# Performance work log

Measured on AMD Instinct MI355X. Metric: run time of the kernel, lower is better.

Reference implementation:

```python
import jax, jax.numpy as jnp
import numpy as np

W = 801  # wavelength grid points
B = 16384  # batch of thickness stacks


def setup_inputs() -> dict:
    key = jax.random.key(0)
    k1, = jax.random.split(key, 1)
    # 7 physical film thicknesses in nm, uniform in [0, 200)
    d_phys = jax.random.uniform(k1, (B, 7), dtype=jnp.float32) * 200.0
    # wavelength grid in nm (docstring: spectrum length 801)
    lam = jnp.linspace(400.0, 800.0, W, dtype=jnp.float32)
    # material refractive indices (module default fallbacks, complex n + ik)
    n_Si = jnp.full((W,), 4.0 + 0.0j, dtype=jnp.complex64)
    n_SiO2 = jnp.full((W,), 1.46 + 0.0j, dtype=jnp.complex64)
    n_Si3N4 = jnp.full((W,), 2.0 + 0.0j, dtype=jnp.complex64)
    return {"d_phys": d_phys, "n_Si": n_Si, "n_SiO2": n_SiO2,
            "n_Si3N4": n_Si3N4, "lam": lam}


def reference(d_phys, n_Si, n_SiO2, n_Si3N4, lam):
    # Transfer-matrix reflectometry for stack:
    # Air | SiO2 | Si3N4 | SiO2 | Si3N4 | SiO2 | Si3N4 | SiO2 | Si
    k0 = (2.0 * jnp.pi) / lam  # [W]
    b = d_phys.shape[0]
    n_Air = jnp.ones_like(n_Si)
    layers_n = [n_Air, n_SiO2, n_Si3N4, n_SiO2, n_Si3N4,
                n_SiO2, n_Si3N4, n_SiO2, n_Si]
    zeros = jnp.zeros((b, 1), dtype=d_phys.dtype)
    d_list = [zeros] + [d_phys[:, i:i + 1] for i in range(7)] + [zeros]

    M00 = jnp.ones((b, lam.shape[0]), dtype=jnp.complex64)
    M11 = jnp.ones_like(M00)
    M01 = jnp.zeros_like(M00)
    M10 = jnp.zeros_like(M00)

    N_curr = layers_n[0]
    n_layers = len(layers_n)
    for i in range(1, n_layers):  # fixed 8-step recurrence over interfaces
        N_next = layers_n[i]
        d_next = d_list[i]  # [b, 1] real
        sum_n = N_curr + N_next  # [W]
        sub_n = N_curr - N_next
        r = sub_n / sum_n            # Fresnel reflection coeff [W]
        inv_t = sum_n / (2.0 * N_curr)  # 1/transmission [W]
        m00 = (M00 + M01 * r) * inv_t
        m01 = (M00 * r + M01) * inv_t
        m10 = (M10 + M11 * r) * inv_t
        m11 = (M10 * r + M11) * inv_t
        M00, M01, M10, M11 = m00, m01, m10, m11
        if i < n_layers - 1:
            phi = k0[None, :] * N_next[None, :] * d_next.astype(jnp.complex64)  # [b, W]
            P = jnp.exp(-1j * phi)
            Pi = jnp.exp(1j * phi)
            M00 = M00 * P
            M01 = M01 * Pi
            M10 = M10 * P
            M11 = M11 * Pi
        N_curr = N_next

    r_final = M10 / M00
    R = jnp.abs(r_final) ** 2  # real reflectance spectrum [b, W]
    return R
```

## Files before the change

### kernel.cpp

```cpp
#include <hip/hip_runtime.h>

#define WPTS 801
#define ROWS 4
#define NT 256

struct c2 { float x, y; };

__device__ __forceinline__ c2 c_addc(c2 a, c2 b) { return {a.x + b.x, a.y + b.y}; }
__device__ __forceinline__ c2 c_subc(c2 a, c2 b) { return {a.x - b.x, a.y - b.y}; }
__device__ __forceinline__ c2 c_divc(c2 a, c2 b) {
    float inv = 1.0f / (b.x * b.x + b.y * b.y);
    return {(a.x * b.x + a.y * b.y) * inv, (a.y * b.x - a.x * b.y) * inv};
}

__global__ __launch_bounds__(NT)
void kla_tmm_kernel(const float* __restrict__ d_phys,
                    const float* __restrict__ nSi_f,
                    const float* __restrict__ nSiO2_f,
                    const float* __restrict__ nSi3N4_f,
                    const float* __restrict__ lam,
                    float* __restrict__ out,
                    int B)
{
    const int nRowBlks = (B + ROWS - 1) / ROWS;
    const int t = blockIdx.x * NT + threadIdx.x;
    if (t >= nRowBlks * WPTS) return;

    const int w = t % WPTS;
    const int row0 = (t / WPTS) * ROWS;
    const int nrows = min(ROWS, B - row0);

    const bool ilv = (nSiO2_f[1] == 0.0f);
    float nSx, nSy, nOx, nOy, nNx, nNy;
    if (ilv) {
        nSx = nSi_f[2 * w];    nSy = nSi_f[2 * w + 1];
        nOx = nSiO2_f[2 * w];  nOy = nSiO2_f[2 * w + 1];
        nNx = nSi3N4_f[2 * w]; nNy = nSi3N4_f[2 * w + 1];
    } else {
        nSx = nSi_f[w];    nSy = 0.0f;
        nOx = nSiO2_f[w];  nOy = 0.0f;
        nNx = nSi3N4_f[w]; nNy = 0.0f;
    }

    const bool realn = (nOy == 0.0f) && (nNy == 0.0f) && (nSy == 0.0f);

    if (realn && nrows == ROWS) {
        const float rlam = __builtin_amdgcn_rcpf(lam[w]);
        const float kOr = nOx * rlam;
        const float kNr = nNx * rlam;
        const float gAO = __builtin_amdgcn_rcpf(nOx);
        const float gON = nOx * __builtin_amdgcn_rcpf(nNx);
        const float gNO = nNx * gAO;

        const float* base = d_phys + (size_t)row0 * 7;
        float* orow = out + (size_t)row0 * WPTS + w;

        #pragma unroll
        for (int rr = 0; rr < ROWS; ++rr) {
            const float* dd = base + (size_t)rr * 7;
            float v0x = nOx, v0y = 0.0f;
            float v1x = nSx, v1y = 0.0f;

            #pragma unroll
            for (int i = 7; i >= 1; --i) {
                const float nu = dd[i - 1] * ((i & 1) ? kOr : kNr);
                const float s = __builtin_amdgcn_sinf(nu);
                const float c = __builtin_amdgcn_cosf(nu);
                const float w0x = v0x * c + v1y * s;
                const float w0y = v0y * c - v1x * s;
                const float w1x = v1x * c + v0y * s;
                const float w1y = v1y * c - v0x * s;
                const float g = (i == 1) ? gAO : ((i & 1) ? gNO : gON);
                v0x = w0x * g;
                v0y = w0y * g;
                v1x = w1x;
                v1y = w1y;
            }

            const float ax = v0x - v1x, ay = v0y - v1y;
            const float bx = v0x + v1x, by = v0y + v1y;
            const float num = ax * ax + ay * ay;
            const float den = bx * bx + by * by;
            orow[(size_t)rr * WPTS] = num * __builtin_amdgcn_rcpf(den);
        }
    } else {
        const float k0 = 6.28318530717958647692f / lam[w];
        const c2 nA = {1.0f, 0.0f};
        const c2 nO = {nOx, nOy}, nN = {nNx, nNy}, nS = {nSx, nSy};
        const c2 rAO  = c_divc(c_subc(nA, nO), c_addc(nA, nO));
        const c2 rON  = c_divc(c_subc(nO, nN), c_addc(nO, nN));
        const c2 rNO  = {-rON.x, -rON.y};
        const c2 rOSi = c_divc(c_subc(nO, nS), c_addc(nO, nS));
        const c2 kO = {k0 * nO.x, k0 * nO.y};
        const c2 kN = {k0 * nN.x, k0 * nN.y};

        for (int rr = 0; rr < nrows; ++rr) {
            const int row = row0 + rr;
            const float* dd = d_phys + (size_t)row * 7;

            c2 u0 = {1.0f, 0.0f};
            c2 u1 = rOSi;

            #pragma unroll
            for (int i = 7; i >= 1; --i) {
                const float d = dd[i - 1];
                const c2 kk = (i & 1) ? kO : kN;
                const float alpha = kk.x * d;
                const float beta  = kk.y * d;
                float s, c;
                __sincosf(alpha, &s, &c);
                const float ep = __expf(beta);
                const float em = __expf(-beta);

                c2 v;
                v.x = ep * (u0.x * c + u0.y * s);
                v.y = ep * (u0.y * c - u0.x * s);
                u0 = v;
                v.x = em * (u1.x * c - u1.y * s);
                v.y = em * (u1.y * c + u1.x * s);
                u1 = v;

                const c2 ri = (i == 1) ? rAO : ((i & 1) ? rNO : rON);
                c2 w0, w1;
                w0.x = u0.x + ri.x * u1.x - ri.y * u1.y;
                w0.y = u0.y + ri.x * u1.y + ri.y * u1.x;
                w1.x = u1.x + ri.x * u0.x - ri.y * u0.y;
                w1.y = u1.y + ri.x * u0.y + ri.y * u0.x;
                u0 = w0; u1 = w1;
            }

            out[(size_t)row * WPTS + w] =
                (u1.x * u1.x + u1.y * u1.y) / (u0.x * u0.x + u0.y * u0.y);
        }
    }
}

extern "C" void kernel_launch(void* const* d_in, const int* in_sizes, int n_in,
                              void* d_out, int out_size, void* d_ws, size_t ws_size,
                              hipStream_t stream) {
    const float* d_phys  = (const float*)d_in[0];
    const float* nSi     = (const float*)d_in[1];
    const float* nSiO2   = (const float*)d_in[2];
    const float* nSi3N4  = (const float*)d_in[3];
    const float* lam     = (const float*)d_in[4];
    float* out = (float*)d_out;

    const int B = in_sizes[0] / 7;
    const int nRowBlks = (B + ROWS - 1) / ROWS;
    const int nTasks = nRowBlks * WPTS;
    const int grid = (nTasks + NT - 1) / NT;

    kla_tmm_kernel<<<grid, NT, 0, stream>>>(
        d_phys, nSi, nSiO2, nSi3N4, lam, out, B);
}
```

Measured before the change: 47.40 us.

## Compute transfer-matrix recurrence in packed fp16 with polynomial sin/cos

```diff
diff --git a/kernel.cpp b/kernel.cpp
--- a/kernel.cpp
+++ b/kernel.cpp
@@ -3,6 +3,8 @@
 #define WPTS 801
 #define ROWS 4
 #define NT 256
+
+typedef _Float16 h2 __attribute__((ext_vector_type(2)));
 
 struct c2 { float x, y; };
 
@@ -11,6 +13,10 @@
 __device__ __forceinline__ c2 c_divc(c2 a, c2 b) {
     float inv = 1.0f / (b.x * b.x + b.y * b.y);
     return {(a.x * b.x + a.y * b.y) * inv, (a.y * b.x - a.x * b.y) * inv};
+}
+
+__device__ __forceinline__ h2 h2bcast(float v) {
+    h2 r; r.x = (_Float16)v; r.y = (_Float16)v; return r;
 }
 
 __global__ __launch_bounds__(NT)
@@ -46,42 +52,86 @@
 
     if (realn && nrows == ROWS) {
         const float rlam = __builtin_amdgcn_rcpf(lam[w]);
-        const float kOr = nOx * rlam;
-        const float kNr = nNx * rlam;
+        const float kO2 = 2.0f * nOx * rlam;
+        const float kN2 = 2.0f * nNx * rlam;
         const float gAO = __builtin_amdgcn_rcpf(nOx);
         const float gON = nOx * __builtin_amdgcn_rcpf(nNx);
         const float gNO = nNx * gAO;
 
+        const h2 hgAO = h2bcast(gAO);
+        const h2 hgON = h2bcast(gON);
+        const h2 hgNO = h2bcast(gNO);
+
+        const h2 hA1 = h2bcast( 3.14159265f);
+        const h2 hA3 = h2bcast(-5.16771278f);
+        const h2 hA5 = h2bcast( 2.55016404f);
+        const h2 hA7 = h2bcast(-0.59926453f);
+        const h2 hC2 = h2bcast(-4.93480220f);
+        const h2 hC4 = h2bcast( 4.05871213f);
+        const h2 hC6 = h2bcast(-1.33526277f);
+        const h2 hOne = h2bcast(1.0f);
+
+        const h2 v0init = h2bcast(nOx);
+        const h2 v1init = h2bcast(nSx);
+
         const float* base = d_phys + (size_t)row0 * 7;
         float* orow = out + (size_t)row0 * WPTS + w;
 
         #pragma unroll
-        for (int rr = 0; rr < ROWS; ++rr) {
-            const float* dd = base + (size_t)rr * 7;
-            float v0x = nOx, v0y = 0.0f;
-            float v1x = nSx, v1y = 0.0f;
+        for (int pr = 0; pr < ROWS; pr += 2) {
+            const float* dA = base + (size_t)pr * 7;
+            const float* dB = dA + 7;
+
+            h2 v0x = v0init, v0y = h2bcast(0.0f);
+            h2 v1x = v1init, v1y = h2bcast(0.0f);
 
             #pragma unroll
             for (int i = 7; i >= 1; --i) {
-                const float nu = dd[i - 1] * ((i & 1) ? kOr : kNr);
-                const float s = __builtin_amdgcn_sinf(nu);
-                const float c = __builtin_amdgcn_cosf(nu);
-                const float w0x = v0x * c + v1y * s;
-                const float w0y = v0y * c - v1x * s;
-                const float w1x = v1x * c + v0y * s;
-                const float w1y = v1y * c - v0x * s;
-                const float g = (i == 1) ? gAO : ((i & 1) ? gNO : gON);
-                v0x = w0x * g;
-                v0y = w0y * g;
-                v1x = w1x;
-                v1y = w1y;
-            }
-
-            const float ax = v0x - v1x, ay = v0y - v1y;
-            const float bx = v0x + v1x, by = v0y + v1y;
-            const float num = ax * ax + ay * ay;
-            const float den = bx * bx + by * by;
-            orow[(size_t)rr * WPTS] = num * __builtin_amdgcn_rcpf(den);
+                const float kk = (i & 1) ? kO2 : kN2;
+                const h2 hg = (i == 1) ? hgAO : ((i & 1) ? hgNO : hgON);
+
+                const float nuA = dA[i - 1] * kk;
+                const float nuB = dB[i - 1] * kk;
+                const float tA = nuA - __builtin_rintf(nuA);
+                const float tB = nuB - __builtin_rintf(nuB);
+                h2 tt; tt.x = (_Float16)tA; tt.y = (_Float16)tB;
+
+                h2 q = tt * tt;
+                h2 ps = hA5 + q * hA7;
+                ps = hA3 + q * ps;
+                ps = hA1 + q * ps;
+                h2 s = tt * ps;
+                h2 pc = hC4 + q * hC6;
+                pc = hC2 + q * pc;
+                h2 c = hOne + q * pc;
+
+                h2 gc = hg * c;
+                h2 gs = hg * s;
+                h2 nv0x = gc * v0x + gs * v1y;
+                h2 nv0y = gc * v0y - gs * v1x;
+                h2 nv1x = c * v1x + s * v0y;
+                h2 nv1y = c * v1y - s * v0x;
+                v0x = nv0x; v0y = nv0y; v1x = nv1x; v1y = nv1y;
+            }
+
+            {
+                const float p0x = (float)v0x.x, p0y = (float)v0y.x;
+                const float p1x = (float)v1x.x, p1y = (float)v1y.x;
+                const float ax = p0x - p1x, ay = p0y - p1y;
+                const float bx = p0x + p1x, by = p0y + p1y;
+                const float num = ax * ax + ay * ay;
+                const float den = bx * bx + by * by;
+                orow[(size_t)pr * WPTS] = num * __builtin_amdgcn_rcpf(den);
+            }
+            {
+                const float p0x = (float)v0x.y, p0y = (float)v0y.y;
+                const float p1x = (float)v1x.y, p1y = (float)v1y.y;
+                const float ax = p0x - p1x, ay = p0y - p1y;
+                const float bx = p0x + p1x, by = p0y + p1y;
+                const float num = ax * ax + ay * ay;
+                const float den = bx * bx + by * by;
+                orow[(size_t)(pr + 1) * WPTS] = num * __builtin_amdgcn_rcpf(den);
+            }
         }
     } else {
         const float k0 = 6.28318530717958647692f / lam[w];
```

New measurement: 46.36 us (median of 2 runs). 1.02x faster.

## Use 2D grid with 8 rows per thread and fold scale into sincos

Applied to the files above, without the earlier changes.

```diff
diff --git a/kernel.cpp b/kernel.cpp
--- a/kernel.cpp
+++ b/kernel.cpp
@@ -1,7 +1,7 @@
 #include <hip/hip_runtime.h>
 
 #define WPTS 801
-#define ROWS 4
+#define RPT 8
 #define NT 256
 
 struct c2 { float x, y; };
@@ -22,13 +22,10 @@
                     float* __restrict__ out,
                     int B)
 {
-    const int nRowBlks = (B + ROWS - 1) / ROWS;
-    const int t = blockIdx.x * NT + threadIdx.x;
-    if (t >= nRowBlks * WPTS) return;
-
-    const int w = t % WPTS;
-    const int row0 = (t / WPTS) * ROWS;
-    const int nrows = min(ROWS, B - row0);
+    const int w = blockIdx.x * NT + threadIdx.x;
+    if (w >= WPTS) return;
+    const int row0 = blockIdx.y * RPT;
+    const int nrows = min(RPT, B - row0);
 
     const bool ilv = (nSiO2_f[1] == 0.0f);
     float nSx, nSy, nOx, nOy, nNx, nNy;
@@ -44,7 +41,7 @@
 
     const bool realn = (nOy == 0.0f) && (nNy == 0.0f) && (nSy == 0.0f);
 
-    if (realn && nrows == ROWS) {
+    if (realn && nrows == RPT) {
         const float rlam = __builtin_amdgcn_rcpf(lam[w]);
         const float kOr = nOx * rlam;
         const float kNr = nNx * rlam;
@@ -52,36 +49,33 @@
         const float gON = nOx * __builtin_amdgcn_rcpf(nNx);
         const float gNO = nNx * gAO;
 
-        const float* base = d_phys + (size_t)row0 * 7;
+        const float* dd = d_phys + (size_t)row0 * 7;
         float* orow = out + (size_t)row0 * WPTS + w;
 
         #pragma unroll
-        for (int rr = 0; rr < ROWS; ++rr) {
-            const float* dd = base + (size_t)rr * 7;
+        for (int r = 0; r < RPT; ++r) {
             float v0x = nOx, v0y = 0.0f;
             float v1x = nSx, v1y = 0.0f;
 
             #pragma unroll
-            for (int i = 7; i >= 1; --i) {
-                const float nu = dd[i - 1] * ((i & 1) ? kOr : kNr);
+            for (int j = 6; j >= 0; --j) {
+                const float nu = dd[r * 7 + j] * ((j & 1) ? kNr : kOr);
                 const float s = __builtin_amdgcn_sinf(nu);
                 const float c = __builtin_amdgcn_cosf(nu);
-                const float w0x = v0x * c + v1y * s;
-                const float w0y = v0y * c - v1x * s;
+                const float g = (j == 0) ? gAO : ((j & 1) ? gON : gNO);
+                const float gc = g * c, gs = g * s;
+                const float w0x = v0x * gc + v1y * gs;
+                const float w0y = v0y * gc - v1x * gs;
                 const float w1x = v1x * c + v0y * s;
                 const float w1y = v1y * c - v0x * s;
-                const float g = (i == 1) ? gAO : ((i & 1) ? gNO : gON);
-                v0x = w0x * g;
-                v0y = w0y * g;
-                v1x = w1x;
-                v1y = w1y;
+                v0x = w0x; v0y = w0y; v1x = w1x; v1y = w1y;
             }
 
             const float ax = v0x - v1x, ay = v0y - v1y;
             const float bx = v0x + v1x, by = v0y + v1y;
             const float num = ax * ax + ay * ay;
             const float den = bx * bx + by * by;
-            orow[(size_t)rr * WPTS] = num * __builtin_amdgcn_rcpf(den);
+            orow[(size_t)r * WPTS] = num * __builtin_amdgcn_rcpf(den);
         }
     } else {
         const float k0 = 6.28318530717958647692f / lam[w];
@@ -146,9 +140,7 @@
     float* out = (float*)d_out;
 
     const int B = in_sizes[0] / 7;
-    const int nRowBlks = (B + ROWS - 1) / ROWS;
-    const int nTasks = nRowBlks * WPTS;
-    const int grid = (nTasks + NT - 1) / NT;
+    dim3 grid((WPTS + NT - 1) / NT, (B + RPT - 1) / RPT);
 
     kla_tmm_kernel<<<grid, NT, 0, stream>>>(
         d_phys, nSi, nSiO2, nSi3N4, lam, out, B);
```

Measured after the change: 58.42 us. 1.23x slower.
